# Performance work log

Hardware: AMD Instinct MI355X
Metric: run time of the kernel (lower is better)

The kernel has to match this reference:

```python
import math
import jax, jax.numpy as jnp
import numpy as np

jax.config.update("jax_enable_x64", True)

P_PRIME = 1000003            # prime modulus; p-1 = 2*3*166667
N_FACTORS = (2, 3, 166667)   # prime factors of p-1 (for primitive-root search)
B, NPATCH, L, K, DIM = 4, 784, 9, 16, 28  # batch, patches/sample, patch len, kernels, map dim


def _modpow(base, exp, p, nbits=21):
    """Vectorized modular exponentiation (square-and-multiply), int64, exponents < 2^nbits."""
    shape = jnp.broadcast_shapes(jnp.shape(base), jnp.shape(exp))
    b0 = jnp.broadcast_to(jnp.asarray(base, jnp.int64) % p, shape)
    e = jnp.broadcast_to(jnp.asarray(exp, jnp.int64), shape)
    def body(i, c):
        res, b = c
        res = jnp.where(((e >> i) & 1) == 1, (res * b) % p, res)
        return (res, (b * b) % p)
    res, _ = jax.lax.fori_loop(0, nbits, body, (jnp.ones(shape, jnp.int64), b0))
    return res


def _decrypt_ips(ct0, cts, y, sk_y, g, p):
    """IPFE decrypt + BSGS discrete log. ct0:[B,P] cts:[B,P,L] y:[K,L] sk_y:[K] -> signed ip [K,B,P]."""
    n = p - 1
    powed = _modpow(cts[None], jnp.mod(y, n)[:, None, None, :], p)   # [K,B,P,L]
    num = powed[..., 0]
    for i in range(1, L):                                            # fixed small L=9
        num = (num * powed[..., i]) % p
    denom = _modpow(ct0[None], jnp.mod(sk_y, n)[:, None, None], p)   # [K,B,P]
    val = (num * _modpow(denom, p - 2, p)) % p                       # = g^{<x,y>} mod p (Fermat inverse)
    # baby-step giant-step over group order n
    m = math.isqrt(n - 1) + 1
    n_giant = -(-n // m)
    baby = _modpow(jnp.int64(g), jnp.arange(m, dtype=jnp.int64), p)  # g^j, j in [0,m)
    order = jnp.argsort(baby)
    sb = baby[order]
    ginv_m = _modpow(jnp.int64(g), jnp.int64((n - m) % n), p)        # g^{-m}
    pt = _modpow(ginv_m, jnp.arange(n_giant, dtype=jnp.int64), p)    # g^{-m*i}
    gamma = (val.reshape(-1)[:, None] * pt[None, :]) % p             # [T, n_giant] giant steps
    pos = jnp.clip(jnp.searchsorted(sb, gamma), 0, m - 1)
    hit = sb[pos] == gamma
    cand = jnp.arange(n_giant, dtype=jnp.int64)[None, :] * m + order[pos]
    ip = jnp.min(jnp.where(hit, cand, n), axis=1)                    # unique match: ip = i*m + j
    ip = jnp.where(ip > n // 2, ip - n, ip)                          # signed representative
    return ip.reshape(K, ct0.shape[0], ct0.shape[1])


def _bn(x, g_, b_, m_, v_):
    s = g_ * jax.lax.rsqrt(v_ + 1e-5)
    return (x - m_[None, :, None, None]) * s[None, :, None, None] + b_[None, :, None, None]


def _conv(x, w, b):
    o = jax.lax.conv_general_dilated(x, w, (1, 1), ((1, 1), (1, 1)),
                                     dimension_numbers=("NCHW", "OIHW", "NCHW"))
    return o + b[None, :, None, None]


def _pool(x):
    return jax.lax.reduce_window(x, jnp.array(-jnp.inf, x.dtype), jax.lax.max,
                                 (1, 1, 2, 2), (1, 1, 2, 2), "VALID")


def _forward(ct0, cts, y, sk_y, bias1, bn1_g, bn1_b, bn1_m, bn1_v,
             conv2_w, conv2_b, bn2_g, bn2_b, bn2_m, bn2_v,
             conv3_w, conv3_b, bn3_g, bn3_b, bn3_m, bn3_v,
             fc1_w, fc1_b, fc2_w, fc2_b, g, p):
    ip = _decrypt_ips(ct0, cts, y, sk_y, g, p)                       # [K,B,P] int64
    maps = ip.astype(jnp.float32) / 10000.0 + bias1[:, None, None]   # dequantize + conv1 bias
    feat = jnp.transpose(maps, (1, 0, 2)).reshape(-1, K, DIM, DIM)   # [B,16,28,28]
    feat = _pool(jax.nn.relu(_bn(feat, bn1_g, bn1_b, bn1_m, bn1_v)))
    feat = _pool(jax.nn.relu(_bn(_conv(feat, conv2_w, conv2_b), bn2_g, bn2_b, bn2_m, bn2_v)))
    feat = _pool(jax.nn.relu(_bn(_conv(feat, conv3_w, conv3_b), bn3_g, bn3_b, bn3_m, bn3_v)))
    flat = feat.reshape(feat.shape[0], -1)                           # [B,576]
    h = jax.nn.relu(flat @ fc1_w.T + fc1_b)                          # dropout = identity (eval mode)
    return h @ fc2_w.T + fc2_b                                       # [B,10]


def setup_inputs():
    rng = np.random.default_rng(0)
    p, n = P_PRIME, P_PRIME - 1
    assert all(p % d for d in range(2, math.isqrt(p) + 1))           # p prime
    g = next(gg for gg in range(2, 200)
             if all(pow(gg, n // q, p) != 1 for q in N_FACTORS))      # primitive root mod p
    s = rng.integers(1, n, size=L)                                    # master secret
    pk = [pow(g, int(si), p) for si in s]
    y = rng.integers(-50, 51, size=(K, L)).astype(np.int64)          # round(w*10000)
    x = rng.integers(0, 21, size=(B, NPATCH, L))                     # quantized patch values
    r = rng.integers(1, n, size=(B, NPATCH))
    gx = [pow(g, t, p) for t in range(21)]
    ct0 = np.zeros((B, NPATCH), dtype=np.int64)
    cts = np.zeros((B, NPATCH, L), dtype=np.int64)
    for b in range(B):
        for j in range(NPATCH):
            rr = int(r[b, j])
            ct0[b, j] = pow(g, rr, p)
            for i in range(L):
                cts[b, j, i] = pow(pk[i], rr, p) * gx[x[b, j, i]] % p
    sk_y = np.array([sum(int(s[i]) * int(y[k, i]) for i in range(L)) % n
                     for k in range(K)], dtype=np.int64)
    f32 = lambda a: jnp.asarray(a, jnp.float32)
    def rn(*sh):
        return f32(rng.standard_normal(sh) * 0.1)
    def bnp(c):
        return (f32(1.0 + 0.1 * rng.standard_normal(c)), rn(c), rn(c), f32(rng.random(c) + 0.5))
    bn1_g, bn1_b, bn1_m, bn1_v = bnp(16)
    bn2_g, bn2_b, bn2_m, bn2_v = bnp(32)
    bn3_g, bn3_b, bn3_m, bn3_v = bnp(64)
    return dict(ct0=jnp.asarray(ct0), cts=jnp.asarray(cts),
                y=jnp.asarray(y), sk_y=jnp.asarray(sk_y), bias1=rn(K),
                bn1_g=bn1_g, bn1_b=bn1_b, bn1_m=bn1_m, bn1_v=bn1_v,
                conv2_w=rn(32, 16, 3, 3), conv2_b=rn(32),
                bn2_g=bn2_g, bn2_b=bn2_b, bn2_m=bn2_m, bn2_v=bn2_v,
                conv3_w=rn(64, 32, 3, 3), conv3_b=rn(64),
                bn3_g=bn3_g, bn3_b=bn3_b, bn3_m=bn3_m, bn3_v=bn3_v,
                fc1_w=rn(128, 576), fc1_b=rn(128),
                fc2_w=rn(10, 128), fc2_b=rn(10), g=g, p=p)


def reference(ct0, cts, y, sk_y, bias1, bn1_g, bn1_b, bn1_m, bn1_v,
              conv2_w, conv2_b, bn2_g, bn2_b, bn2_m, bn2_v,
              conv3_w, conv3_b, bn3_g, bn3_b, bn3_m, bn3_v,
              fc1_w, fc1_b, fc2_w, fc2_b, g, p):
    return _forward(ct0, cts, y, sk_y, bias1, bn1_g, bn1_b, bn1_m, bn1_v,
                    conv2_w, conv2_b, bn2_g, bn2_b, bn2_m, bn2_v,
                    conv3_w, conv3_b, bn3_g, bn3_b, bn3_m, bn3_v,
                    fc1_w, fc1_b, fc2_w, fc2_b, g, p)
```

## Files before the change

kernel.cpp:

```cpp
#include <hip/hip_runtime.h>
#include <stdint.h>

#define PRIME 1000003u
#define NORD  1000002u
#define KCH   16
#define BATCH 4
#define NPATCH 784
#define LLEN  9
#define IPMAX 9000
#define TBLN  (2*IPMAX+1)
#define NDEC  (KCH*BATCH*NPATCH)

__device__ __forceinline__ uint32_t mmul(uint32_t a, uint32_t b) {
    uint64_t t = (uint64_t)a * (uint64_t)b;
    uint32_t q = (uint32_t)((t * 2199016ull) >> 41);
    uint32_t r = (uint32_t)t - q * PRIME;
    return (r >= PRIME) ? r - PRIME : r;
}

__device__ __forceinline__ uint32_t mpow(uint32_t base, uint32_t exp) {
    uint32_t r = 1u, b = base;
    while (exp) {
        if (exp & 1u) r = mmul(r, b);
        b = mmul(b, b);
        exp >>= 1;
    }
    return r;
}

__global__ void build_table(const int* __restrict__ g_in, int16_t* __restrict__ table) {
    int e = blockIdx.x * blockDim.x + threadIdx.x;
    if (e >= TBLN) return;
    int es = e - IPMAX;
    uint32_t exp = (es >= 0) ? (uint32_t)es : (uint32_t)(es + (int)NORD);
    table[mpow((uint32_t)g_in[0], exp)] = (int16_t)es;
}

__global__ void __launch_bounds__(256) decrypt(
    const int* __restrict__ ct0, const int* __restrict__ cts,
    const int* __restrict__ y, const int* __restrict__ sk_y,
    const float* __restrict__ bias1,
    const float* __restrict__ bn1_g, const float* __restrict__ bn1_b,
    const float* __restrict__ bn1_m, const float* __restrict__ bn1_v,
    const int16_t* __restrict__ table, float* __restrict__ featr) {
    int gtid = blockIdx.x * 256 + threadIdx.x;
    if (gtid >= NDEC) return;
    int k = __builtin_amdgcn_readfirstlane(gtid / (BATCH * NPATCH));
    int r = gtid % (BATCH * NPATCH);
    int b = r / NPATCH;
    int j = r % NPATCH;

    const int* crow = cts + ((b * NPATCH) + j) * LLEN;
    const int* yrow = y + k * LLEN;

    uint32_t c[LLEN];
    int yv[LLEN];
#pragma unroll
    for (int i = 0; i < LLEN; i++) {
        yv[i] = yrow[i];
        c[i]  = (uint32_t)crow[i];
    }

    uint32_t accp = 1u, accn = 1u;
#pragma unroll
    for (int bit = 5; bit >= 0; bit--) {
        accp = mmul(accp, accp);
        accn = mmul(accn, accn);
#pragma unroll
        for (int i = 0; i < LLEN; i++) {
            int yi = yv[i];
            int ay = (yi > 0) ? yi : -yi;
            if ((ay >> bit) & 1) {
                if (yi > 0) accp = mmul(accp, c[i]);
                else        accn = mmul(accn, c[i]);
            }
        }
    }

    uint32_t den = mpow((uint32_t)ct0[b * NPATCH + j], (uint32_t)sk_y[k]);
    den = mmul(den, accn);
    uint32_t val = mmul(accp, mpow(den, PRIME - 2u));

    int ip = (int)table[val];

    float sc = bn1_g[k] * rsqrtf(bn1_v[k] + 1e-5f);
    float shf = (bias1[k] - bn1_m[k]) * sc + bn1_b[k];
    float v_ = fmaf((float)ip, sc * 1e-4f, shf);
    featr[((b * KCH) + k) * NPATCH + j] = fmaxf(v_, 0.0f);
}

__global__ void __launch_bounds__(256) conv2_k(
    const float* __restrict__ featr,
    const float* __restrict__ conv2_w, const float* __restrict__ conv2_b,
    const float* __restrict__ bn2_g, const float* __restrict__ bn2_b,
    const float* __restrict__ bn2_m, const float* __restrict__ bn2_v,
    float* __restrict__ s2g) {
    const int b  = blockIdx.x >> 5;
    const int oc = blockIdx.x & 31;
    const int tid = threadIdx.x;

    __shared__ float s1p[16][16][16];
    __shared__ float w[16 * 9];
    __shared__ float co[196];

    for (int i = tid; i < 16 * 16 * 16; i += 256)
        ((float*)s1p)[i] = 0.0f;
    if (tid < 144) w[tid] = conv2_w[oc * 144 + tid];
    __syncthreads();
    for (int i = tid; i < 16 * 196; i += 256) {
        int ic = i / 196, pos = i % 196;
        int yy = pos / 14, xx = pos % 14;
        const float* fp = featr + ((b * 16 + ic) * 784) + (2 * yy) * 28 + 2 * xx;
        s1p[ic][yy + 1][xx + 1] = fmaxf(fmaxf(fp[0], fp[1]), fmaxf(fp[28], fp[29]));
    }
    __syncthreads();

    if (tid < 196) {
        int oh = tid / 14, ow = tid % 14;
        float a0 = 0.0f, a1 = 0.0f, a2 = 0.0f;
#pragma unroll
        for (int ic = 0; ic < 16; ic++) {
            const float* wp = &w[ic * 9];
            const float* sp = &s1p[ic][oh][ow];
            a0 = fmaf(sp[0],  wp[0], fmaf(sp[1],  wp[1], fmaf(sp[2],  wp[2], a0)));
            a1 = fmaf(sp[16], wp[3], fmaf(sp[17], wp[4], fmaf(sp[18], wp[5], a1)));
            a2 = fmaf(sp[32], wp[6], fmaf(sp[33], wp[7], fmaf(sp[34], wp[8], a2)));
        }
        float sc = bn2_g[oc] * rsqrtf(bn2_v[oc] + 1e-5f);
        float shf = bn2_b[oc] - bn2_m[oc] * sc;
        co[tid] = fmaxf((a0 + a1 + a2 + conv2_b[oc]) * sc + shf, 0.0f);
    }
    __syncthreads();

    if (tid < 49) {
        int oh = tid / 7, ow = tid % 7;
        const float* c0 = &co[(2 * oh) * 14 + 2 * ow];
        s2g[((b * 32 + oc) * 49) + tid] =
            fmaxf(fmaxf(c0[0], c0[1]), fmaxf(c0[14], c0[15]));
    }
}

__global__ void __launch_bounds__(64) conv3_k(
    const float* __restrict__ s2g,
    const float* __restrict__ conv3_w, const float* __restrict__ conv3_b,
    const float* __restrict__ bn3_g, const float* __restrict__ bn3_b,
    const float* __restrict__ bn3_m, const float* __restrict__ bn3_v,
    float* __restrict__ s3g) {
    const int b  = blockIdx.x >> 6;
    const int oc = blockIdx.x & 63;
    const int tid = threadIdx.x;

    __shared__ float s2p[32][9][9];
    __shared__ float w[32 * 9];
    __shared__ float co[49];

    for (int i = tid; i < 32 * 81; i += 64)
        ((float*)s2p)[i] = 0.0f;
    for (int i = tid; i < 288; i += 64) w[i] = conv3_w[oc * 288 + i];
    __syncthreads();
    for (int i = tid; i < 32 * 49; i += 64) {
        int ic = i / 49, pos = i % 49;
        s2p[ic][pos / 7 + 1][pos % 7 + 1] = s2g[((b * 32 + ic) * 49) + pos];
    }
    __syncthreads();

    if (tid < 49) {
        int oh = tid / 7, ow = tid % 7;
        float a0 = 0.0f, a1 = 0.0f, a2 = 0.0f;
#pragma unroll
        for (int ic = 0; ic < 32; ic++) {
            const float* wp = &w[ic * 9];
            const float* sp = &s2p[ic][oh][ow];
            a0 = fmaf(sp[0],  wp[0], fmaf(sp[1],  wp[1], fmaf(sp[2],  wp[2], a0)));
            a1 = fmaf(sp[9],  wp[3], fmaf(sp[10], wp[4], fmaf(sp[11], wp[5], a1)));
            a2 = fmaf(sp[18], wp[6], fmaf(sp[19], wp[7], fmaf(sp[20], wp[8], a2)));
        }
        float sc = bn3_g[oc] * rsqrtf(bn3_v[oc] + 1e-5f);
        float shf = bn3_b[oc] - bn3_m[oc] * sc;
        co[tid] = fmaxf((a0 + a1 + a2 + conv3_b[oc]) * sc + shf, 0.0f);
    }
    __syncthreads();

    if (tid < 9) {
        int oh = tid / 3, ow = tid % 3;
        const float* c0 = &co[(2 * oh) * 7 + 2 * ow];
        s3g[b * 576 + oc * 9 + tid] = fmaxf(fmaxf(c0[0], c0[1]), fmaxf(c0[7], c0[8]));
    }
}

__global__ void __launch_bounds__(1024) fc_k(
    const float* __restrict__ s3g,
    const float* __restrict__ fc1_w, const float* __restrict__ fc1_b,
    const float* __restrict__ fc2_w, const float* __restrict__ fc2_b,
    float* __restrict__ out) {
    const int b = blockIdx.x;
    const int tid = threadIdx.x;
    const int wid = tid >> 6, lane = tid & 63;
    __shared__ float s3[576];
    __shared__ float h[128];

    for (int i = tid; i < 576; i += 1024) s3[i] = s3g[b * 576 + i];
    __syncthreads();

#pragma unroll
    for (int oo = 0; oo < 8; oo++) {
        int o = wid * 8 + oo;
        const float* w = fc1_w + o * 576;
        float acc = 0.0f;
#pragma unroll
        for (int jj = 0; jj < 9; jj++)
            acc = fmaf(s3[jj * 64 + lane], w[jj * 64 + lane], acc);
#pragma unroll
        for (int off = 32; off; off >>= 1) acc += __shfl_down(acc, off);
        if (lane == 0) h[o] = fmaxf(acc + fc1_b[o], 0.0f);
    }
    __syncthreads();

    if (wid < 10) {
        const float* w = fc2_w + wid * 128;
        float acc = fmaf(h[lane], w[lane], 0.0f);
        acc = fmaf(h[64 + lane], w[64 + lane], acc);
#pragma unroll
        for (int off = 32; off; off >>= 1) acc += __shfl_down(acc, off);
        if (lane == 0) out[b * 10 + wid] = acc + fc2_b[wid];
    }
}

extern "C" void kernel_launch(void* const* d_in, const int* in_sizes, int n_in,
                              void* d_out, int out_size, void* d_ws, size_t ws_size,
                              hipStream_t stream) {
    const int*   ct0    = (const int*)d_in[0];
    const int*   cts    = (const int*)d_in[1];
    const int*   y      = (const int*)d_in[2];
    const int*   sk_y   = (const int*)d_in[3];
    const float* bias1  = (const float*)d_in[4];
    const float* bn1_g  = (const float*)d_in[5];
    const float* bn1_b  = (const float*)d_in[6];
    const float* bn1_m  = (const float*)d_in[7];
    const float* bn1_v  = (const float*)d_in[8];
    const float* conv2_w = (const float*)d_in[9];
    const float* conv2_b = (const float*)d_in[10];
    const float* bn2_g  = (const float*)d_in[11];
    const float* bn2_b  = (const float*)d_in[12];
    const float* bn2_m  = (const float*)d_in[13];
    const float* bn2_v  = (const float*)d_in[14];
    const float* conv3_w = (const float*)d_in[15];
    const float* conv3_b = (const float*)d_in[16];
    const float* bn3_g  = (const float*)d_in[17];
    const float* bn3_b  = (const float*)d_in[18];
    const float* bn3_m  = (const float*)d_in[19];
    const float* bn3_v  = (const float*)d_in[20];
    const float* fc1_w  = (const float*)d_in[21];
    const float* fc1_b  = (const float*)d_in[22];
    const float* fc2_w  = (const float*)d_in[23];
    const float* fc2_b  = (const float*)d_in[24];
    const int*   g_in   = (const int*)d_in[25];
    float* out = (float*)d_out;

    char* ws = (char*)d_ws;
    int16_t* table = (int16_t*)ws;
    float* featr = (float*)(ws + 2000128);
    float* s2g   = (float*)(ws + 2200832);
    float* s3g   = (float*)(ws + 2225920);

    build_table<<<(TBLN + 255) / 256, 256, 0, stream>>>(g_in, table);

    decrypt<<<NDEC / 256, 256, 0, stream>>>(
        ct0, cts, y, sk_y, bias1, bn1_g, bn1_b, bn1_m, bn1_v, table, featr);

    conv2_k<<<BATCH * 32, 256, 0, stream>>>(
        featr, conv2_w, conv2_b, bn2_g, bn2_b, bn2_m, bn2_v, s2g);

    conv3_k<<<BATCH * 64, 64, 0, stream>>>(
        s2g, conv3_w, conv3_b, bn3_g, bn3_b, bn3_m, bn3_v, s3g);

    fc_k<<<BATCH, 1024, 0, stream>>>(s3g, fc1_w, fc1_b, fc2_w, fc2_b, out);
}
```

Baseline: 144.0 us.

## Fuse decrypt, conv2, conv3 and FC into one persistent kernel with grid barriers

Replaces the four kernels after table construction with one 196-block kernel that runs each stage in turn, separated by atomic-counter grid barriers. The counter is reset by build_table. Conv3 now computes four output channels per 256-thread block, and the FC stage uses 256 threads instead of 1024. This removes three kernel launch gaps. In exchange it relies on all 196 blocks being co-resident, spin-waits at each barrier, and leaves FC with less parallelism.

```diff
diff --git a/kernel.cpp b/kernel.cpp
--- a/kernel.cpp
+++ b/kernel.cpp
@@ -10,6 +10,7 @@
 #define IPMAX 9000
 #define TBLN  (2*IPMAX+1)
 #define NDEC  (KCH*BATCH*NPATCH)
+#define NBLK  196
 
 __device__ __forceinline__ uint32_t mmul(uint32_t a, uint32_t b) {
     uint64_t t = (uint64_t)a * (uint64_t)b;
@@ -28,201 +29,217 @@
     return r;
 }
 
-__global__ void build_table(const int* __restrict__ g_in, int16_t* __restrict__ table) {
+__device__ __forceinline__ void gridbar(unsigned* ctr, unsigned target) {
+    __syncthreads();
+    if (threadIdx.x == 0) {
+        __hip_atomic_fetch_add(ctr, 1u, __ATOMIC_RELEASE, __HIP_MEMORY_SCOPE_AGENT);
+        while (__hip_atomic_load(ctr, __ATOMIC_ACQUIRE, __HIP_MEMORY_SCOPE_AGENT) < target)
+            __builtin_amdgcn_s_sleep(2);
+    }
+    __syncthreads();
+}
+
+__global__ void build_table(const int* __restrict__ g_in, int16_t* __restrict__ table,
+                            unsigned* __restrict__ ctr) {
     int e = blockIdx.x * blockDim.x + threadIdx.x;
     if (e >= TBLN) return;
+    if (e == 0) *ctr = 0u;
     int es = e - IPMAX;
     uint32_t exp = (es >= 0) ? (uint32_t)es : (uint32_t)(es + (int)NORD);
     table[mpow((uint32_t)g_in[0], exp)] = (int16_t)es;
 }
 
-__global__ void __launch_bounds__(256) decrypt(
+__global__ void __launch_bounds__(256) fused(
     const int* __restrict__ ct0, const int* __restrict__ cts,
     const int* __restrict__ y, const int* __restrict__ sk_y,
     const float* __restrict__ bias1,
     const float* __restrict__ bn1_g, const float* __restrict__ bn1_b,
     const float* __restrict__ bn1_m, const float* __restrict__ bn1_v,
-    const int16_t* __restrict__ table, float* __restrict__ featr) {
-    int gtid = blockIdx.x * 256 + threadIdx.x;
-    if (gtid >= NDEC) return;
-    int k = __builtin_amdgcn_readfirstlane(gtid / (BATCH * NPATCH));
-    int r = gtid % (BATCH * NPATCH);
-    int b = r / NPATCH;
-    int j = r % NPATCH;
-
-    const int* crow = cts + ((b * NPATCH) + j) * LLEN;
-    const int* yrow = y + k * LLEN;
-
-    uint32_t c[LLEN];
-    int yv[LLEN];
-#pragma unroll
-    for (int i = 0; i < LLEN; i++) {
-        yv[i] = yrow[i];
-        c[i]  = (uint32_t)crow[i];
-    }
-
-    uint32_t accp = 1u, accn = 1u;
-#pragma unroll
-    for (int bit = 5; bit >= 0; bit--) {
-        accp = mmul(accp, accp);
-        accn = mmul(accn, accn);
-#pragma unroll
-        for (int i = 0; i < LLEN; i++) {
-            int yi = yv[i];
-            int ay = (yi > 0) ? yi : -yi;
-            if ((ay >> bit) & 1) {
-                if (yi > 0) accp = mmul(accp, c[i]);
-                else        accn = mmul(accn, c[i]);
-            }
-        }
-    }
-
-    uint32_t den = mpow((uint32_t)ct0[b * NPATCH + j], (uint32_t)sk_y[k]);
-    den = mmul(den, accn);
-    uint32_t val = mmul(accp, mpow(den, PRIME - 2u));
-
-    int ip = (int)table[val];
-
-    float sc = bn1_g[k] * rsqrtf(bn1_v[k] + 1e-5f);
-    float shf = (bias1[k] - bn1_m[k]) * sc + bn1_b[k];
-    float v_ = fmaf((float)ip, sc * 1e-4f, shf);
-    featr[((b * KCH) + k) * NPATCH + j] = fmaxf(v_, 0.0f);
-}
-
-__global__ void __launch_bounds__(256) conv2_k(
-    const float* __restrict__ featr,
     const float* __restrict__ conv2_w, const float* __restrict__ conv2_b,
     const float* __restrict__ bn2_g, const float* __restrict__ bn2_b,
     const float* __restrict__ bn2_m, const float* __restrict__ bn2_v,
-    float* __restrict__ s2g) {
-    const int b  = blockIdx.x >> 5;
-    const int oc = blockIdx.x & 31;
-    const int tid = threadIdx.x;
-
-    __shared__ float s1p[16][16][16];
-    __shared__ float w[16 * 9];
-    __shared__ float co[196];
-
-    for (int i = tid; i < 16 * 16 * 16; i += 256)
-        ((float*)s1p)[i] = 0.0f;
-    if (tid < 144) w[tid] = conv2_w[oc * 144 + tid];
-    __syncthreads();
-    for (int i = tid; i < 16 * 196; i += 256) {
-        int ic = i / 196, pos = i % 196;
-        int yy = pos / 14, xx = pos % 14;
-        const float* fp = featr + ((b * 16 + ic) * 784) + (2 * yy) * 28 + 2 * xx;
-        s1p[ic][yy + 1][xx + 1] = fmaxf(fmaxf(fp[0], fp[1]), fmaxf(fp[28], fp[29]));
-    }
-    __syncthreads();
-
-    if (tid < 196) {
-        int oh = tid / 14, ow = tid % 14;
-        float a0 = 0.0f, a1 = 0.0f, a2 = 0.0f;
-#pragma unroll
-        for (int ic = 0; ic < 16; ic++) {
-            const float* wp = &w[ic * 9];
-            const float* sp = &s1p[ic][oh][ow];
-            a0 = fmaf(sp[0],  wp[0], fmaf(sp[1],  wp[1], fmaf(sp[2],  wp[2], a0)));
-            a1 = fmaf(sp[16], wp[3], fmaf(sp[17], wp[4], fmaf(sp[18], wp[5], a1)));
-            a2 = fmaf(sp[32], wp[6], fmaf(sp[33], wp[7], fmaf(sp[34], wp[8], a2)));
-        }
-        float sc = bn2_g[oc] * rsqrtf(bn2_v[oc] + 1e-5f);
-        float shf = bn2_b[oc] - bn2_m[oc] * sc;
-        co[tid] = fmaxf((a0 + a1 + a2 + conv2_b[oc]) * sc + shf, 0.0f);
-    }
-    __syncthreads();
-
-    if (tid < 49) {
-        int oh = tid / 7, ow = tid % 7;
-        const float* c0 = &co[(2 * oh) * 14 + 2 * ow];
-        s2g[((b * 32 + oc) * 49) + tid] =
-            fmaxf(fmaxf(c0[0], c0[1]), fmaxf(c0[14], c0[15]));
-    }
-}
-
-__global__ void __launch_bounds__(64) conv3_k(
-    const float* __restrict__ s2g,
     const float* __restrict__ conv3_w, const float* __restrict__ conv3_b,
     const float* __restrict__ bn3_g, const float* __restrict__ bn3_b,
     const float* __restrict__ bn3_m, const float* __restrict__ bn3_v,
-    float* __restrict__ s3g) {
-    const int b  = blockIdx.x >> 6;
-    const int oc = blockIdx.x & 63;
-    const int tid = threadIdx.x;
-
-    __shared__ float s2p[32][9][9];
-    __shared__ float w[32 * 9];
-    __shared__ float co[49];
-
-    for (int i = tid; i < 32 * 81; i += 64)
-        ((float*)s2p)[i] = 0.0f;
-    for (int i = tid; i < 288; i += 64) w[i] = conv3_w[oc * 288 + i];
-    __syncthreads();
-    for (int i = tid; i < 32 * 49; i += 64) {
-        int ic = i / 49, pos = i % 49;
-        s2p[ic][pos / 7 + 1][pos % 7 + 1] = s2g[((b * 32 + ic) * 49) + pos];
-    }
-    __syncthreads();
-
-    if (tid < 49) {
-        int oh = tid / 7, ow = tid % 7;
-        float a0 = 0.0f, a1 = 0.0f, a2 = 0.0f;
-#pragma unroll
-        for (int ic = 0; ic < 32; ic++) {
-            const float* wp = &w[ic * 9];
-            const float* sp = &s2p[ic][oh][ow];
-            a0 = fmaf(sp[0],  wp[0], fmaf(sp[1],  wp[1], fmaf(sp[2],  wp[2], a0)));
-            a1 = fmaf(sp[9],  wp[3], fmaf(sp[10], wp[4], fmaf(sp[11], wp[5], a1)));
-            a2 = fmaf(sp[18], wp[6], fmaf(sp[19], wp[7], fmaf(sp[20], wp[8], a2)));
-        }
-        float sc = bn3_g[oc] * rsqrtf(bn3_v[oc] + 1e-5f);
-        float shf = bn3_b[oc] - bn3_m[oc] * sc;
-        co[tid] = fmaxf((a0 + a1 + a2 + conv3_b[oc]) * sc + shf, 0.0f);
-    }
-    __syncthreads();
-
-    if (tid < 9) {
-        int oh = tid / 3, ow = tid % 3;
-        const float* c0 = &co[(2 * oh) * 7 + 2 * ow];
-        s3g[b * 576 + oc * 9 + tid] = fmaxf(fmaxf(c0[0], c0[1]), fmaxf(c0[7], c0[8]));
-    }
-}
-
-__global__ void __launch_bounds__(1024) fc_k(
-    const float* __restrict__ s3g,
     const float* __restrict__ fc1_w, const float* __restrict__ fc1_b,
     const float* __restrict__ fc2_w, const float* __restrict__ fc2_b,
-    float* __restrict__ out) {
-    const int b = blockIdx.x;
+    const int16_t* __restrict__ table,
+    float* __restrict__ featr, float* __restrict__ s2g, float* __restrict__ s3g,
+    float* __restrict__ out, unsigned* __restrict__ ctr) {
+
+    __shared__ union {
+        struct { float s1p[16][16][16]; float w[144]; float co[196]; } c2;
+        struct { float s2p[32][9][9];  float w[4][288]; float co[4][49]; } c3;
+        struct { float s3[576]; float h[128]; } fc;
+    } sm;
+
+    const int bid = blockIdx.x;
     const int tid = threadIdx.x;
-    const int wid = tid >> 6, lane = tid & 63;
-    __shared__ float s3[576];
-    __shared__ float h[128];
-
-    for (int i = tid; i < 576; i += 1024) s3[i] = s3g[b * 576 + i];
-    __syncthreads();
-
-#pragma unroll
-    for (int oo = 0; oo < 8; oo++) {
-        int o = wid * 8 + oo;
-        const float* w = fc1_w + o * 576;
-        float acc = 0.0f;
-#pragma unroll
-        for (int jj = 0; jj < 9; jj++)
-            acc = fmaf(s3[jj * 64 + lane], w[jj * 64 + lane], acc);
-#pragma unroll
-        for (int off = 32; off; off >>= 1) acc += __shfl_down(acc, off);
-        if (lane == 0) h[o] = fmaxf(acc + fc1_b[o], 0.0f);
-    }
-    __syncthreads();
-
-    if (wid < 10) {
-        const float* w = fc2_w + wid * 128;
-        float acc = fmaf(h[lane], w[lane], 0.0f);
-        acc = fmaf(h[64 + lane], w[64 + lane], acc);
-#pragma unroll
-        for (int off = 32; off; off >>= 1) acc += __shfl_down(acc, off);
-        if (lane == 0) out[b * 10 + wid] = acc + fc2_b[wid];
+
+    {
+        int gtid = bid * 256 + tid;
+        int k = __builtin_amdgcn_readfirstlane(gtid / (BATCH * NPATCH));
+        int r = gtid % (BATCH * NPATCH);
+        int b = r / NPATCH;
+        int j = r % NPATCH;
+
+        const int* crow = cts + ((b * NPATCH) + j) * LLEN;
+        const int* yrow = y + k * LLEN;
+
+        uint32_t c[LLEN];
+        int yv[LLEN];
+#pragma unroll
+        for (int i = 0; i < LLEN; i++) {
+            yv[i] = yrow[i];
+            c[i]  = (uint32_t)crow[i];
+        }
+
+        uint32_t accp = 1u, accn = 1u;
+#pragma unroll
+        for (int bit = 5; bit >= 0; bit--) {
+            accp = mmul(accp, accp);
+            accn = mmul(accn, accn);
+#pragma unroll
+            for (int i = 0; i < LLEN; i++) {
+                int yi = yv[i];
+                int ay = (yi > 0) ? yi : -yi;
+                if ((ay >> bit) & 1) {
+                    if (yi > 0) accp = mmul(accp, c[i]);
+                    else        accn = mmul(accn, c[i]);
+                }
+            }
+        }
+
+        uint32_t den = mpow((uint32_t)ct0[b * NPATCH + j], (uint32_t)sk_y[k]);
+        den = mmul(den, accn);
+        uint32_t val = mmul(accp, mpow(den, PRIME - 2u));
+
+        int ip = (int)table[val];
+
+        float sc = bn1_g[k] * rsqrtf(bn1_v[k] + 1e-5f);
+        float shf = (bias1[k] - bn1_m[k]) * sc + bn1_b[k];
+        float v_ = fmaf((float)ip, sc * 1e-4f, shf);
+        featr[((b * KCH) + k) * NPATCH + j] = fmaxf(v_, 0.0f);
+    }
+
+    gridbar(ctr, NBLK);
+
+    if (bid < 128) {
+        const int b  = bid >> 5;
+        const int oc = bid & 31;
+
+        for (int i = tid; i < 16 * 16 * 16; i += 256)
+            ((float*)sm.c2.s1p)[i] = 0.0f;
+        if (tid < 144) sm.c2.w[tid] = conv2_w[oc * 144 + tid];
+        __syncthreads();
+        for (int i = tid; i < 16 * 196; i += 256) {
+            int ic = i / 196, pos = i % 196;
+            int yy = pos / 14, xx = pos % 14;
+            const float* fp = featr + ((b * 16 + ic) * 784) + (2 * yy) * 28 + 2 * xx;
+            sm.c2.s1p[ic][yy + 1][xx + 1] = fmaxf(fmaxf(fp[0], fp[1]), fmaxf(fp[28], fp[29]));
+        }
+        __syncthreads();
+
+        if (tid < 196) {
+            int oh = tid / 14, ow = tid % 14;
+            float a0 = 0.0f, a1 = 0.0f, a2 = 0.0f;
+#pragma unroll
+            for (int ic = 0; ic < 16; ic++) {
+                const float* wp = &sm.c2.w[ic * 9];
+                const float* sp = &sm.c2.s1p[ic][oh][ow];
+                a0 = fmaf(sp[0],  wp[0], fmaf(sp[1],  wp[1], fmaf(sp[2],  wp[2], a0)));
+                a1 = fmaf(sp[16], wp[3], fmaf(sp[17], wp[4], fmaf(sp[18], wp[5], a1)));
+                a2 = fmaf(sp[32], wp[6], fmaf(sp[33], wp[7], fmaf(sp[34], wp[8], a2)));
+            }
+            float sc = bn2_g[oc] * rsqrtf(bn2_v[oc] + 1e-5f);
+            float shf = bn2_b[oc] - bn2_m[oc] * sc;
+            sm.c2.co[tid] = fmaxf((a0 + a1 + a2 + conv2_b[oc]) * sc + shf, 0.0f);
+        }
+        __syncthreads();
+
+        if (tid < 49) {
+            int oh = tid / 7, ow = tid % 7;
+            const float* c0 = &sm.c2.co[(2 * oh) * 14 + 2 * ow];
+            s2g[((b * 32 + oc) * 49) + tid] =
+                fmaxf(fmaxf(c0[0], c0[1]), fmaxf(c0[14], c0[15]));
+        }
+    }
+
+    gridbar(ctr, 2 * NBLK);
+
+    if (bid < 64) {
+        const int b = bid >> 4, ocg = bid & 15;
+
+        for (int i = tid; i < 32 * 81; i += 256)
+            ((float*)sm.c3.s2p)[i] = 0.0f;
+        for (int i = tid; i < 4 * 288; i += 256) {
+            int w2 = i / 288, rr = i % 288;
+            sm.c3.w[w2][rr] = conv3_w[(ocg * 4 + w2) * 288 + rr];
+        }
+        __syncthreads();
+        for (int i = tid; i < 32 * 49; i += 256) {
+            int ic = i / 49, pos = i % 49;
+            sm.c3.s2p[ic][pos / 7 + 1][pos % 7 + 1] = s2g[((b * 32 + ic) * 49) + pos];
+        }
+        __syncthreads();
+
+        const int wid = tid >> 6, lane = tid & 63;
+        if (lane < 49) {
+            int oh = lane / 7, ow = lane % 7;
+            float a0 = 0.0f, a1 = 0.0f, a2 = 0.0f;
+#pragma unroll
+            for (int ic = 0; ic < 32; ic++) {
+                const float* wp = &sm.c3.w[wid][ic * 9];
+                const float* sp = &sm.c3.s2p[ic][oh][ow];
+                a0 = fmaf(sp[0],  wp[0], fmaf(sp[1],  wp[1], fmaf(sp[2],  wp[2], a0)));
+                a1 = fmaf(sp[9],  wp[3], fmaf(sp[10], wp[4], fmaf(sp[11], wp[5], a1)));
+                a2 = fmaf(sp[18], wp[6], fmaf(sp[19], wp[7], fmaf(sp[20], wp[8], a2)));
+            }
+            int oc = ocg * 4 + wid;
+            float sc = bn3_g[oc] * rsqrtf(bn3_v[oc] + 1e-5f);
+            float shf = bn3_b[oc] - bn3_m[oc] * sc;
+            sm.c3.co[wid][lane] = fmaxf((a0 + a1 + a2 + conv3_b[oc]) * sc + shf, 0.0f);
+        }
+        __syncthreads();
+
+        if (tid < 36) {
+            int w2 = tid / 9, p = tid % 9;
+            int oh = p / 3, ow = p % 3;
+            const float* c0 = &sm.c3.co[w2][(2 * oh) * 7 + 2 * ow];
+            s3g[b * 576 + (ocg * 4 + w2) * 9 + p] =
+                fmaxf(fmaxf(c0[0], c0[1]), fmaxf(c0[7], c0[8]));
+        }
+    }
+
+    gridbar(ctr, 3 * NBLK);
+
+    if (bid < BATCH) {
+        const int b = bid;
+        for (int i = tid; i < 576; i += 256) sm.fc.s3[i] = s3g[b * 576 + i];
+        __syncthreads();
+
+        const int wid = tid >> 6, lane = tid & 63;
+        for (int oo = 0; oo < 32; oo++) {
+            int o = wid * 32 + oo;
+            const float* w = fc1_w + o * 576;
+            float acc = 0.0f;
+#pragma unroll
+            for (int jj = 0; jj < 9; jj++)
+                acc = fmaf(sm.fc.s3[jj * 64 + lane], w[jj * 64 + lane], acc);
+#pragma unroll
+            for (int off = 32; off; off >>= 1) acc += __shfl_down(acc, off);
+            if (lane == 0) sm.fc.h[o] = fmaxf(acc + fc1_b[o], 0.0f);
+        }
+        __syncthreads();
+
+        for (int o = wid; o < 10; o += 4) {
+            const float* w = fc2_w + o * 128;
+            float acc = fmaf(sm.fc.h[lane], w[lane], 0.0f);
+            acc = fmaf(sm.fc.h[64 + lane], w[64 + lane], acc);
+#pragma unroll
+            for (int off = 32; off; off >>= 1) acc += __shfl_down(acc, off);
+            if (lane == 0) out[b * 10 + o] = acc + fc2_b[o];
+        }
     }
 }
 
@@ -258,21 +275,17 @@
     float* out = (float*)d_out;
 
     char* ws = (char*)d_ws;
-    int16_t* table = (int16_t*)ws;
+    int16_t*  table = (int16_t*)ws;
+    unsigned* ctr   = (unsigned*)(ws + 2000064);
     float* featr = (float*)(ws + 2000128);
     float* s2g   = (float*)(ws + 2200832);
     float* s3g   = (float*)(ws + 2225920);
 
-    build_table<<<(TBLN + 255) / 256, 256, 0, stream>>>(g_in, table);
-
-    decrypt<<<NDEC / 256, 256, 0, stream>>>(
-        ct0, cts, y, sk_y, bias1, bn1_g, bn1_b, bn1_m, bn1_v, table, featr);
-
-    conv2_k<<<BATCH * 32, 256, 0, stream>>>(
-        featr, conv2_w, conv2_b, bn2_g, bn2_b, bn2_m, bn2_v, s2g);
-
-    conv3_k<<<BATCH * 64, 64, 0, stream>>>(
-        s2g, conv3_w, conv3_b, bn3_g, bn3_b, bn3_m, bn3_v, s3g);
-
-    fc_k<<<BATCH, 1024, 0, stream>>>(s3g, fc1_w, fc1_b, fc2_w, fc2_b, out);
-}
+    build_table<<<(TBLN + 255) / 256, 256, 0, stream>>>(g_in, table, ctr);
+
+    fused<<<NBLK, 256, 0, stream>>>(
+        ct0, cts, y, sk_y, bias1, bn1_g, bn1_b, bn1_m, bn1_v,
+        conv2_w, conv2_b, bn2_g, bn2_b, bn2_m, bn2_v,
+        conv3_w, conv3_b, bn3_g, bn3_b, bn3_m, bn3_v,
+        fc1_w, fc1_b, fc2_w, fc2_b, table, featr, s2g, s3g, out, ctr);
+}
```

New measurement: 181.8 us. +26.2%, slower.

## Fuse first max-pool into decrypt and merge conv2, conv3 and FC into one kernel

Applied to the files above, without the earlier changes.

The decrypt kernel now runs one block per half image per channel and writes a 2x2 max-pooled map, which shrinks the intermediate buffer. The conv2, conv3 and two fully connected layers become a single kernel with one 1024-thread block per batch sample. Intermediates stay in shared memory, and the union reuses that space across stages. This removes three kernel launches and their global round-trips, at the cost of running the whole tail of the network on only 4 blocks with serial loops over channel groups.

```diff
diff --git a/kernel.cpp b/kernel.cpp
--- a/kernel.cpp
+++ b/kernel.cpp
@@ -9,7 +9,8 @@
 #define LLEN  9
 #define IPMAX 9000
 #define TBLN  (2*IPMAX+1)
-#define NDEC  (KCH*BATCH*NPATCH)
+
+#define POOL_OFF 2000128
 
 __device__ __forceinline__ uint32_t mmul(uint32_t a, uint32_t b) {
     uint64_t t = (uint64_t)a * (uint64_t)b;
@@ -36,175 +37,158 @@
     table[mpow((uint32_t)g_in[0], exp)] = (int16_t)es;
 }
 
-__global__ void __launch_bounds__(256) decrypt(
+__global__ void __launch_bounds__(448) decrypt_pool(
     const int* __restrict__ ct0, const int* __restrict__ cts,
     const int* __restrict__ y, const int* __restrict__ sk_y,
     const float* __restrict__ bias1,
     const float* __restrict__ bn1_g, const float* __restrict__ bn1_b,
     const float* __restrict__ bn1_m, const float* __restrict__ bn1_v,
-    const int16_t* __restrict__ table, float* __restrict__ featr) {
-    int gtid = blockIdx.x * 256 + threadIdx.x;
-    if (gtid >= NDEC) return;
-    int k = __builtin_amdgcn_readfirstlane(gtid / (BATCH * NPATCH));
-    int r = gtid % (BATCH * NPATCH);
-    int b = r / NPATCH;
-    int j = r % NPATCH;
-
-    const int* crow = cts + ((b * NPATCH) + j) * LLEN;
+    const int16_t* __restrict__ table, float* __restrict__ pooled) {
+    __shared__ float raw[392];
+    const int bid = blockIdx.x, tid = threadIdx.x;
+    const int pair = bid >> 1, half = bid & 1;
+    const int k = pair & 15, b = pair >> 4;
+
     const int* yrow = y + k * LLEN;
-
-    uint32_t c[LLEN];
     int yv[LLEN];
 #pragma unroll
-    for (int i = 0; i < LLEN; i++) {
-        yv[i] = yrow[i];
-        c[i]  = (uint32_t)crow[i];
-    }
-
-    uint32_t accp = 1u, accn = 1u;
-#pragma unroll
-    for (int bit = 5; bit >= 0; bit--) {
-        accp = mmul(accp, accp);
-        accn = mmul(accn, accn);
-#pragma unroll
-        for (int i = 0; i < LLEN; i++) {
-            int yi = yv[i];
-            int ay = (yi > 0) ? yi : -yi;
-            if ((ay >> bit) & 1) {
-                if (yi > 0) accp = mmul(accp, c[i]);
-                else        accn = mmul(accn, c[i]);
+    for (int i = 0; i < LLEN; i++) yv[i] = yrow[i];
+    const uint32_t sk = (uint32_t)sk_y[k];
+    const float sc  = bn1_g[k] * rsqrtf(bn1_v[k] + 1e-5f);
+    const float shf = (bias1[k] - bn1_m[k]) * sc + bn1_b[k];
+
+    if (tid < 392) {
+        const int j = half * 392 + tid;
+        const int* crow = cts + ((b * NPATCH) + j) * LLEN;
+        uint32_t c[LLEN];
+#pragma unroll
+        for (int i = 0; i < LLEN; i++) c[i] = (uint32_t)crow[i];
+
+        uint32_t accp = 1u, accn = 1u;
+#pragma unroll
+        for (int bit = 5; bit >= 0; bit--) {
+            accp = mmul(accp, accp);
+            accn = mmul(accn, accn);
+#pragma unroll
+            for (int i = 0; i < LLEN; i++) {
+                int yi = yv[i];
+                int ay = (yi > 0) ? yi : -yi;
+                if ((ay >> bit) & 1) {
+                    if (yi > 0) accp = mmul(accp, c[i]);
+                    else        accn = mmul(accn, c[i]);
+                }
             }
         }
-    }
-
-    uint32_t den = mpow((uint32_t)ct0[b * NPATCH + j], (uint32_t)sk_y[k]);
-    den = mmul(den, accn);
-    uint32_t val = mmul(accp, mpow(den, PRIME - 2u));
-
-    int ip = (int)table[val];
-
-    float sc = bn1_g[k] * rsqrtf(bn1_v[k] + 1e-5f);
-    float shf = (bias1[k] - bn1_m[k]) * sc + bn1_b[k];
-    float v_ = fmaf((float)ip, sc * 1e-4f, shf);
-    featr[((b * KCH) + k) * NPATCH + j] = fmaxf(v_, 0.0f);
-}
-
-__global__ void __launch_bounds__(256) conv2_k(
-    const float* __restrict__ featr,
+
+        uint32_t den = mmul(mpow((uint32_t)ct0[b * NPATCH + j], sk), accn);
+        uint32_t val = mmul(accp, mpow(den, PRIME - 2u));
+
+        int ip = (int)table[val];
+        raw[tid] = fmaxf(fmaf((float)ip, sc * 1e-4f, shf), 0.0f);
+    }
+    __syncthreads();
+    if (tid < 98) {
+        int pyl = tid / 14, px = tid % 14;
+        const float* r0 = &raw[(2 * pyl) * 28 + 2 * px];
+        float m = fmaxf(fmaxf(r0[0], r0[1]), fmaxf(r0[28], r0[29]));
+        pooled[((b * KCH) + k) * 196 + (half * 7 + pyl) * 14 + px] = m;
+    }
+}
+
+__global__ void __launch_bounds__(1024) convnet(
+    const float* __restrict__ pooled,
     const float* __restrict__ conv2_w, const float* __restrict__ conv2_b,
     const float* __restrict__ bn2_g, const float* __restrict__ bn2_b,
     const float* __restrict__ bn2_m, const float* __restrict__ bn2_v,
-    float* __restrict__ s2g) {
-    const int b  = blockIdx.x >> 5;
-    const int oc = blockIdx.x & 31;
-    const int tid = threadIdx.x;
-
-    __shared__ float s1p[16][16][16];
-    __shared__ float w[16 * 9];
-    __shared__ float co[196];
-
-    for (int i = tid; i < 16 * 16 * 16; i += 256)
-        ((float*)s1p)[i] = 0.0f;
-    if (tid < 144) w[tid] = conv2_w[oc * 144 + tid];
-    __syncthreads();
-    for (int i = tid; i < 16 * 196; i += 256) {
-        int ic = i / 196, pos = i % 196;
-        int yy = pos / 14, xx = pos % 14;
-        const float* fp = featr + ((b * 16 + ic) * 784) + (2 * yy) * 28 + 2 * xx;
-        s1p[ic][yy + 1][xx + 1] = fmaxf(fmaxf(fp[0], fp[1]), fmaxf(fp[28], fp[29]));
-    }
-    __syncthreads();
-
-    if (tid < 196) {
-        int oh = tid / 14, ow = tid % 14;
-        float a0 = 0.0f, a1 = 0.0f, a2 = 0.0f;
-#pragma unroll
-        for (int ic = 0; ic < 16; ic++) {
-            const float* wp = &w[ic * 9];
-            const float* sp = &s1p[ic][oh][ow];
-            a0 = fmaf(sp[0],  wp[0], fmaf(sp[1],  wp[1], fmaf(sp[2],  wp[2], a0)));
-            a1 = fmaf(sp[16], wp[3], fmaf(sp[17], wp[4], fmaf(sp[18], wp[5], a1)));
-            a2 = fmaf(sp[32], wp[6], fmaf(sp[33], wp[7], fmaf(sp[34], wp[8], a2)));
-        }
-        float sc = bn2_g[oc] * rsqrtf(bn2_v[oc] + 1e-5f);
-        float shf = bn2_b[oc] - bn2_m[oc] * sc;
-        co[tid] = fmaxf((a0 + a1 + a2 + conv2_b[oc]) * sc + shf, 0.0f);
-    }
-    __syncthreads();
-
-    if (tid < 49) {
-        int oh = tid / 7, ow = tid % 7;
-        const float* c0 = &co[(2 * oh) * 14 + 2 * ow];
-        s2g[((b * 32 + oc) * 49) + tid] =
-            fmaxf(fmaxf(c0[0], c0[1]), fmaxf(c0[14], c0[15]));
-    }
-}
-
-__global__ void __launch_bounds__(64) conv3_k(
-    const float* __restrict__ s2g,
     const float* __restrict__ conv3_w, const float* __restrict__ conv3_b,
     const float* __restrict__ bn3_g, const float* __restrict__ bn3_b,
     const float* __restrict__ bn3_m, const float* __restrict__ bn3_v,
-    float* __restrict__ s3g) {
-    const int b  = blockIdx.x >> 6;
-    const int oc = blockIdx.x & 63;
-    const int tid = threadIdx.x;
-
-    __shared__ float s2p[32][9][9];
-    __shared__ float w[32 * 9];
-    __shared__ float co[49];
-
-    for (int i = tid; i < 32 * 81; i += 64)
-        ((float*)s2p)[i] = 0.0f;
-    for (int i = tid; i < 288; i += 64) w[i] = conv3_w[oc * 288 + i];
-    __syncthreads();
-    for (int i = tid; i < 32 * 49; i += 64) {
-        int ic = i / 49, pos = i % 49;
-        s2p[ic][pos / 7 + 1][pos % 7 + 1] = s2g[((b * 32 + ic) * 49) + pos];
-    }
-    __syncthreads();
-
-    if (tid < 49) {
-        int oh = tid / 7, ow = tid % 7;
-        float a0 = 0.0f, a1 = 0.0f, a2 = 0.0f;
-#pragma unroll
-        for (int ic = 0; ic < 32; ic++) {
-            const float* wp = &w[ic * 9];
-            const float* sp = &s2p[ic][oh][ow];
-            a0 = fmaf(sp[0],  wp[0], fmaf(sp[1],  wp[1], fmaf(sp[2],  wp[2], a0)));
-            a1 = fmaf(sp[9],  wp[3], fmaf(sp[10], wp[4], fmaf(sp[11], wp[5], a1)));
-            a2 = fmaf(sp[18], wp[6], fmaf(sp[19], wp[7], fmaf(sp[20], wp[8], a2)));
-        }
-        float sc = bn3_g[oc] * rsqrtf(bn3_v[oc] + 1e-5f);
-        float shf = bn3_b[oc] - bn3_m[oc] * sc;
-        co[tid] = fmaxf((a0 + a1 + a2 + conv3_b[oc]) * sc + shf, 0.0f);
-    }
-    __syncthreads();
-
-    if (tid < 9) {
-        int oh = tid / 3, ow = tid % 3;
-        const float* c0 = &co[(2 * oh) * 7 + 2 * ow];
-        s3g[b * 576 + oc * 9 + tid] = fmaxf(fmaxf(c0[0], c0[1]), fmaxf(c0[7], c0[8]));
-    }
-}
-
-__global__ void __launch_bounds__(1024) fc_k(
-    const float* __restrict__ s3g,
     const float* __restrict__ fc1_w, const float* __restrict__ fc1_b,
     const float* __restrict__ fc2_w, const float* __restrict__ fc2_b,
     float* __restrict__ out) {
-    const int b = blockIdx.x;
-    const int tid = threadIdx.x;
+    const int b = blockIdx.x, tid = threadIdx.x;
+
+    __shared__ float s2p[32][9][9];
+    __shared__ float s3[576];
+    __shared__ union {
+        struct { float s1p[16][16][16]; float w2[32 * 144]; float co[4][196]; } a;
+        struct { float w3[16 * 288]; float co3[16][49]; } c;
+        struct { float h[128]; } d;
+    } sm;
+
+    for (int i = tid; i < 16 * 16 * 16; i += 1024) ((float*)sm.a.s1p)[i] = 0.0f;
+    for (int i = tid; i < 32 * 81;      i += 1024) ((float*)s2p)[i] = 0.0f;
+    for (int i = tid; i < 32 * 144;     i += 1024) sm.a.w2[i] = conv2_w[i];
+    __syncthreads();
+    for (int i = tid; i < 16 * 196; i += 1024) {
+        int ic = i / 196, pos = i % 196;
+        sm.a.s1p[ic][pos / 14 + 1][pos % 14 + 1] = pooled[(b * KCH + ic) * 196 + pos];
+    }
+    __syncthreads();
+
+    for (int g = 0; g < 8; ++g) {
+        if (tid < 784) {
+            int ocs = tid / 196, pos = tid % 196;
+            int oh = pos / 14, ow = pos % 14;
+            int oc = g * 4 + ocs;
+            float a0 = 0.0f, a1 = 0.0f, a2 = 0.0f;
+#pragma unroll
+            for (int ic = 0; ic < 16; ic++) {
+                const float* wp = &sm.a.w2[oc * 144 + ic * 9];
+                const float* sp = &sm.a.s1p[ic][oh][ow];
+                a0 = fmaf(sp[0],  wp[0], fmaf(sp[1],  wp[1], fmaf(sp[2],  wp[2], a0)));
+                a1 = fmaf(sp[16], wp[3], fmaf(sp[17], wp[4], fmaf(sp[18], wp[5], a1)));
+                a2 = fmaf(sp[32], wp[6], fmaf(sp[33], wp[7], fmaf(sp[34], wp[8], a2)));
+            }
+            float sc = bn2_g[oc] * rsqrtf(bn2_v[oc] + 1e-5f);
+            float shf = bn2_b[oc] - bn2_m[oc] * sc;
+            sm.a.co[ocs][pos] = fmaxf((a0 + a1 + a2 + conv2_b[oc]) * sc + shf, 0.0f);
+        }
+        __syncthreads();
+        if (tid < 196) {
+            int ocs = tid / 49, pp = tid % 49;
+            int oh = pp / 7, ow = pp % 7;
+            const float* c0 = &sm.a.co[ocs][(2 * oh) * 14 + 2 * ow];
+            s2p[g * 4 + ocs][oh + 1][ow + 1] =
+                fmaxf(fmaxf(c0[0], c0[1]), fmaxf(c0[14], c0[15]));
+        }
+        __syncthreads();
+    }
+
+    for (int g = 0; g < 4; ++g) {
+        for (int i = tid; i < 16 * 288; i += 1024)
+            sm.c.w3[i] = conv3_w[g * 16 * 288 + i];
+        __syncthreads();
+        if (tid < 784) {
+            int ocs = tid / 49, pos = tid % 49;
+            int oh = pos / 7, ow = pos % 7;
+            int oc = g * 16 + ocs;
+            float a0 = 0.0f, a1 = 0.0f, a2 = 0.0f;
+#pragma unroll
+            for (int ic = 0; ic < 32; ic++) {
+                const float* wp = &sm.c.w3[ocs * 288 + ic * 9];
+                const float* sp = &s2p[ic][oh][ow];
+                a0 = fmaf(sp[0],  wp[0], fmaf(sp[1],  wp[1], fmaf(sp[2],  wp[2], a0)));
+                a1 = fmaf(sp[9],  wp[3], fmaf(sp[10], wp[4], fmaf(sp[11], wp[5], a1)));
+                a2 = fmaf(sp[18], wp[6], fmaf(sp[19], wp[7], fmaf(sp[20], wp[8], a2)));
+            }
+            float sc = bn3_g[oc] * rsqrtf(bn3_v[oc] + 1e-5f);
+            float shf = bn3_b[oc] - bn3_m[oc] * sc;
+            sm.c.co3[ocs][pos] = fmaxf((a0 + a1 + a2 + conv3_b[oc]) * sc + shf, 0.0f);
+        }
+        __syncthreads();
+        if (tid < 144) {
+            int ocs = tid / 9, pp = tid % 9;
+            int oh = pp / 3, ow = pp % 3;
+            const float* c0 = &sm.c.co3[ocs][(2 * oh) * 7 + 2 * ow];
+            s3[(g * 16 + ocs) * 9 + pp] =
+                fmaxf(fmaxf(c0[0], c0[1]), fmaxf(c0[7], c0[8]));
+        }
+        __syncthreads();
+    }
+
     const int wid = tid >> 6, lane = tid & 63;
-    __shared__ float s3[576];
-    __shared__ float h[128];
-
-    for (int i = tid; i < 576; i += 1024) s3[i] = s3g[b * 576 + i];
-    __syncthreads();
-
-#pragma unroll
-    for (int oo = 0; oo < 8; oo++) {
-        int o = wid * 8 + oo;
+    for (int o = wid; o < 128; o += 16) {
         const float* w = fc1_w + o * 576;
         float acc = 0.0f;
 #pragma unroll
@@ -212,14 +196,14 @@
             acc = fmaf(s3[jj * 64 + lane], w[jj * 64 + lane], acc);
 #pragma unroll
         for (int off = 32; off; off >>= 1) acc += __shfl_down(acc, off);
-        if (lane == 0) h[o] = fmaxf(acc + fc1_b[o], 0.0f);
+        if (lane == 0) sm.d.h[o] = fmaxf(acc + fc1_b[o], 0.0f);
     }
     __syncthreads();
 
     if (wid < 10) {
         const float* w = fc2_w + wid * 128;
-        float acc = fmaf(h[lane], w[lane], 0.0f);
-        acc = fmaf(h[64 + lane], w[64 + lane], acc);
+        float acc = fmaf(sm.d.h[lane], w[lane], 0.0f);
+        acc = fmaf(sm.d.h[64 + lane], w[64 + lane], acc);
 #pragma unroll
         for (int off = 32; off; off >>= 1) acc += __shfl_down(acc, off);
         if (lane == 0) out[b * 10 + wid] = acc + fc2_b[wid];
@@ -258,21 +242,16 @@
     float* out = (float*)d_out;
 
     char* ws = (char*)d_ws;
-    int16_t* table = (int16_t*)ws;
-    float* featr = (float*)(ws + 2000128);
-    float* s2g   = (float*)(ws + 2200832);
-    float* s3g   = (float*)(ws + 2225920);
+    int16_t* table  = (int16_t*)ws;
+    float*   pooled = (float*)(ws + POOL_OFF);
 
     build_table<<<(TBLN + 255) / 256, 256, 0, stream>>>(g_in, table);
 
-    decrypt<<<NDEC / 256, 256, 0, stream>>>(
-        ct0, cts, y, sk_y, bias1, bn1_g, bn1_b, bn1_m, bn1_v, table, featr);
-
-    conv2_k<<<BATCH * 32, 256, 0, stream>>>(
-        featr, conv2_w, conv2_b, bn2_g, bn2_b, bn2_m, bn2_v, s2g);
-
-    conv3_k<<<BATCH * 64, 64, 0, stream>>>(
-        s2g, conv3_w, conv3_b, bn3_g, bn3_b, bn3_m, bn3_v, s3g);
-
-    fc_k<<<BATCH, 1024, 0, stream>>>(s3g, fc1_w, fc1_b, fc2_w, fc2_b, out);
-}
+    decrypt_pool<<<128, 448, 0, stream>>>(
+        ct0, cts, y, sk_y, bias1, bn1_g, bn1_b, bn1_m, bn1_v, table, pooled);
+
+    convnet<<<BATCH, 1024, 0, stream>>>(
+        pooled, conv2_w, conv2_b, bn2_g, bn2_b, bn2_m, bn2_v,
+        conv3_w, conv3_b, bn3_g, bn3_b, bn3_m, bn3_v,
+        fc1_w, fc1_b, fc2_w, fc2_b, out);
+}
```

Result: slower. 221.9 us (+54.0%).
